# Performance work log

Measured on AMD Instinct MI355X. Metric: run time of the kernel, lower is better.

Reference implementation:

```python
import jax, jax.numpy as jnp
import numpy as np

B, T, C = 2, 1024, 2048
E, TOPK = 8, 2
F_MOE = 1408
F_SHARED = 5632


def setup_inputs() -> dict:
    key = jax.random.key(0)
    ks = jax.random.split(key, 9)
    s = 0.02
    return {
        "x": jax.random.normal(ks[0], (B, T, C), dtype=jnp.float32),
        "gate_w": jax.random.normal(ks[1], (E, C), dtype=jnp.float32) * s,
        "expert_fc1": jax.random.normal(ks[2], (E, F_MOE, C), dtype=jnp.float32) * s,
        "expert_fc2": jax.random.normal(ks[3], (E, F_MOE, C), dtype=jnp.float32) * s,
        "expert_proj": jax.random.normal(ks[4], (E, C, F_MOE), dtype=jnp.float32) * s,
        "shared_fc1": jax.random.normal(ks[5], (F_SHARED, C), dtype=jnp.float32) * s,
        "shared_fc2": jax.random.normal(ks[6], (F_SHARED, C), dtype=jnp.float32) * s,
        "shared_proj": jax.random.normal(ks[7], (C, F_SHARED), dtype=jnp.float32) * s,
        "shared_gate_w": jax.random.normal(ks[8], (1, C), dtype=jnp.float32) * s,
    }


def reference(x, gate_w, expert_fc1, expert_fc2, expert_proj,
              shared_fc1, shared_fc2, shared_proj, shared_gate_w):
    b, t, c = x.shape
    xf = x.reshape(-1, c)                                   # [N, C]
    n = xf.shape[0]

    # router: softmax in fp32, then top-k
    router = xf @ gate_w.T                                  # [N, E]
    probs = jax.nn.softmax(router.astype(jnp.float32), axis=1).astype(x.dtype)
    top_p, top_i = jax.lax.top_k(probs, TOPK)               # [N, k]

    # dense combine weights: prob where selected else 0 (top-k indices are distinct)
    combine = jnp.zeros((n, E), dtype=x.dtype).at[
        jnp.arange(n)[:, None], top_i].set(top_p)            # [N, E]

    # per-expert SwiGLU MLP, computed densely then weighted by combine
    h1 = jnp.einsum('nc,efc->enf', xf, expert_fc1)          # [E, N, F]
    h2 = jnp.einsum('nc,efc->enf', xf, expert_fc2)
    h = jax.nn.silu(h1) * h2
    out_e = jnp.einsum('enf,ecf->enc', h, expert_proj)      # [E, N, C]
    y = jnp.einsum('ne,enc->nc', combine, out_e)            # [N, C]

    # shared expert with sigmoid gate
    s1 = xf @ shared_fc1.T
    s2 = xf @ shared_fc2.T
    shared = (jax.nn.silu(s1) * s2) @ shared_proj.T         # [N, C]
    y = y + jax.nn.sigmoid(xf @ shared_gate_w.T) * shared
    return y.reshape(b, t, c)
```

## Files before the change

kernel.cpp:

```cpp
#include <hip/hip_runtime.h>
#include <hip/hip_bf16.h>
#include <math.h>
#include <stdint.h>

#define N_TOK   2048
#define C_DIM   2048
#define E_NUM   8
#define F_MOE   1408
#define F_SH    5632
#define SLOTS   4096
#define PADROWS 4608

typedef __bf16 bf16;
typedef __bf16 bf16x8 __attribute__((ext_vector_type(8)));
typedef __bf16 bf16x4 __attribute__((ext_vector_type(4)));
typedef float  f32x4  __attribute__((ext_vector_type(4)));

__device__ __forceinline__ f32x4 mfma16(bf16x8 a, bf16x8 b, f32x4 c) {
    return __builtin_amdgcn_mfma_f32_16x16x32_bf16(a, b, c, 0, 0, 0);
}
__device__ __forceinline__ void gload16(const void* g, void* l) {
    __builtin_amdgcn_global_load_lds(
        (const __attribute__((address_space(1))) void*)g,
        (__attribute__((address_space(3))) void*)l, 16, 0, 0);
}
#define RAWBAR()  asm volatile("s_barrier" ::: "memory")
#define VMCNT12() asm volatile("s_waitcnt vmcnt(12)" ::: "memory")
#define VMCNT8()  asm volatile("s_waitcnt vmcnt(8)" ::: "memory")
#define VMCNT4()  asm volatile("s_waitcnt vmcnt(4)" ::: "memory")
#define VMCNT0()  asm volatile("s_waitcnt vmcnt(0)" ::: "memory")

__global__ void router_kernel(const float* __restrict__ x,
                              const float* __restrict__ gate_w,
                              const float* __restrict__ sgate_w,
                              int* __restrict__ slotexp,
                              float* __restrict__ slotp,
                              float* __restrict__ sig)
{
    const int n   = blockIdx.x;
    const int tid = threadIdx.x;
    const float* xr = x + (size_t)n * C_DIM;
    const int c0 = tid * 8;

    float xv[8];
#pragma unroll
    for (int j = 0; j < 8; ++j) xv[j] = xr[c0 + j];

    float dots[9];
#pragma unroll
    for (int e = 0; e < 9; ++e) {
        const float* wr = (e < 8) ? (gate_w + (size_t)e * C_DIM) : sgate_w;
        float p = 0.f;
#pragma unroll
        for (int j = 0; j < 8; ++j) p += xv[j] * wr[c0 + j];
#pragma unroll
        for (int off = 32; off > 0; off >>= 1) p += __shfl_down(p, off);
        dots[e] = p;
    }

    __shared__ float red[4][9];
    const int wid = tid >> 6, lane = tid & 63;
    if (lane == 0) {
#pragma unroll
        for (int e = 0; e < 9; ++e) red[wid][e] = dots[e];
    }
    __syncthreads();
    if (tid == 0) {
        float l[9];
#pragma unroll
        for (int e = 0; e < 9; ++e)
            l[e] = red[0][e] + red[1][e] + red[2][e] + red[3][e];
        float mx = l[0];
#pragma unroll
        for (int e = 1; e < 8; ++e) mx = fmaxf(mx, l[e]);
        float p[8], s = 0.f;
#pragma unroll
        for (int e = 0; e < 8; ++e) { p[e] = expf(l[e] - mx); s += p[e]; }
        const float inv = 1.f / s;
#pragma unroll
        for (int e = 0; e < 8; ++e) p[e] *= inv;
        int i1 = 0;
#pragma unroll
        for (int e = 1; e < 8; ++e) if (p[e] > p[i1]) i1 = e;
        int i2 = (i1 == 0) ? 1 : 0;
#pragma unroll
        for (int e = 0; e < 8; ++e) if (e != i1 && p[e] > p[i2]) i2 = e;
        slotexp[2 * n]     = i1;  slotp[2 * n]     = p[i1];
        slotexp[2 * n + 1] = i2;  slotp[2 * n + 1] = p[i2];
        sig[n] = 1.f / (1.f + expf(-l[8]));
    }
}

__global__ void scatter_kernel(const int* __restrict__ slotexp,
                               int* __restrict__ counts, int* __restrict__ bases,
                               int* __restrict__ pos_of, int* __restrict__ row_token)
{
    const int tid = threadIdx.x;
    const int w = tid >> 6, lane = tid & 63;
    __shared__ int cnt[E_NUM], base[E_NUM];

    int run = 0;
    for (int s0 = 0; s0 < SLOTS; s0 += 64) {
        int e = slotexp[s0 + lane];
        unsigned long long m = __ballot(e == w);
        run += __popcll(m);
    }
    if (lane == 0) cnt[w] = run;
    __syncthreads();
    if (tid == 0) {
        int b = 0;
        for (int e = 0; e < E_NUM; ++e) { base[e] = b; b += cnt[e]; }
    }
    __syncthreads();
    run = 0;
    for (int s0 = 0; s0 < SLOTS; s0 += 64) {
        const int s = s0 + lane;
        const int e = slotexp[s];
        unsigned long long m = __ballot(e == w);
        if (e == w) {
            const unsigned long long lt = (lane == 0) ? 0ull : (~0ull >> (64 - lane));
            const int pos = base[w] + run + __popcll(m & lt);
            pos_of[s]      = pos;
            row_token[pos] = s >> 1;
        }
        run += __popcll(m);
    }
    if (lane == 0) { counts[w] = cnt[w]; bases[w] = base[w]; }
}

struct CvtArgs {
    const float* in[5];
    bf16*        out[5];
    int          cum[6];
};

__global__ void cvt_all_kernel(CvtArgs a)
{
    int b = blockIdx.x;
    int s = 0;
#pragma unroll
    for (int k = 1; k < 5; ++k) s += (b >= a.cum[k]);
    const size_t base = (size_t)(b - a.cum[s]) * 8192;
    const float* in = a.in[s];
    bf16* out = a.out[s];
    const int t4 = threadIdx.x * 4;
    f32x4 v[8];
#pragma unroll
    for (int c = 0; c < 8; ++c)
        v[c] = __builtin_nontemporal_load((const f32x4*)(in + base + c * 1024 + t4));
#pragma unroll
    for (int c = 0; c < 8; ++c) {
        bf16x4 o;
#pragma unroll
        for (int j = 0; j < 4; ++j) o[j] = (bf16)v[c][j];
        __builtin_nontemporal_store(o, (bf16x4*)(out + base + c * 1024 + t4));
    }
}

__global__ void gather_kernel(const bf16* __restrict__ Xs,
                              const int* __restrict__ row_token,
                              bf16* __restrict__ Xg)
{
    const int pos = blockIdx.x;
    const int t   = row_token[pos];
    const bf16x8* s = (const bf16x8*)(Xs + (size_t)t * C_DIM);
    bf16x8*       d = (bf16x8*)(Xg + (size_t)pos * C_DIM);
    d[threadIdx.x] = s[threadIdx.x];
}

template<bool DUAL, int KSPLIT>
__device__ __forceinline__ void gemm_body(
    const bf16* __restrict__ A, int lda,
    const bf16* __restrict__ B1g, const bf16* __restrict__ B2g, size_t strideB,
    bf16* __restrict__ OUTh, bf16* __restrict__ OUTq, int ldo, size_t strideOut,
    int base, int cnt, int e, int yt, int nt, int kp, int K, char* lds)
{
    const int KT = (K / 64) / KSPLIT;
    const int H  = 2 * KT;

    const int m0 = base + yt * 256;
    const int tid = threadIdx.x;
    const int w = tid >> 6, lane = tid & 63;

    const int l3  = lane >> 3;
    const int chS = (lane & 7) ^ l3;
    const int hiS = chS >> 2, ccS = chS & 3;
    const int rl  = w * 16 + 2 * l3 + hiS;
    const size_t lda2 = (size_t)lda * 2, K2 = (size_t)K * 2;
    const size_t kpoff = (size_t)kp * KT * 128;

    const char* aSrc0 = (const char*)A + (size_t)(m0 + rl)       * lda2 + ccS * 16 + kpoff;
    const char* aSrc1 = (const char*)A + (size_t)(m0 + 128 + rl) * lda2 + ccS * 16 + kpoff;
    const bf16* B1 = B1g + (size_t)e * strideB;
    const char* bSrc0;
    const char* bSrc1;
    if constexpr (DUAL) {
        const bf16* B2 = B2g + (size_t)e * strideB;
        bSrc0 = (const char*)B1 + (size_t)(nt * 128 + rl) * K2 + ccS * 16 + kpoff;
        bSrc1 = (const char*)B2 + (size_t)(nt * 128 + rl) * K2 + ccS * 16 + kpoff;
    } else {
        bSrc0 = (const char*)B1 + (size_t)(nt * 256 + rl)       * K2 + ccS * 16 + kpoff;
        bSrc1 = (const char*)B1 + (size_t)(nt * 256 + 128 + rl) * K2 + ccS * 16 + kpoff;
    }
    char* ldsw = lds + w * 1024;

    auto issue = [&](int h, int buf) {
        const size_t ko = (size_t)(h >> 1) * 128 + (size_t)(h & 1) * 64;
        char* d = ldsw + buf * 32768;
        gload16(aSrc0 + ko, d);
        gload16(aSrc1 + ko, d + 8192);
        gload16(bSrc0 + ko, d + 16384);
        gload16(bSrc1 + ko, d + 24576);
    };

    const int wm = w >> 2, wn = w & 3;
    const int fr = lane & 15, fq = lane >> 4;
    const int chRd = (((fr & 1) << 2) | fq) ^ ((fr >> 1) & 7);
    uint32_t aOff[8], bOff[4];
#pragma unroll
    for (int m = 0; m < 8; ++m)
        aOff[m] = (uint32_t)((wm * 64 + m * 8 + (fr >> 1)) * 128 + chRd * 16);
#pragma unroll
    for (int n = 0; n < 4; ++n) {
        int rp;
        if constexpr (DUAL)
            rp = (n < 2) ? (wn * 16 + n * 8) : (64 + wn * 16 + (n - 2) * 8);
        else
            rp = wn * 32 + n * 8;
        rp += (fr >> 1);
        bOff[n] = (uint32_t)(16384 + rp * 128 + chRd * 16);
    }

    f32x4 acc[8][4] = {};

    auto compute_half = [&](int buf) {
        const char* LB = lds + buf * 32768;
        bf16x8 af[4], ag[4], bf[4];
#pragma unroll
        for (int n = 0; n < 4; ++n) bf[n] = *(const bf16x8*)(LB + bOff[n]);
#pragma unroll
        for (int m = 0; m < 4; ++m) af[m] = *(const bf16x8*)(LB + aOff[m]);
#pragma unroll
        for (int m = 0; m < 4; ++m) ag[m] = *(const bf16x8*)(LB + aOff[4 + m]);
        __builtin_amdgcn_s_setprio(1);
#pragma unroll
        for (int m = 0; m < 4; ++m)
#pragma unroll
            for (int n = 0; n < 4; ++n)
                acc[m][n] = mfma16(af[m], bf[n], acc[m][n]);
#pragma unroll
        for (int m = 0; m < 4; ++m)
#pragma unroll
            for (int n = 0; n < 4; ++n)
                acc[4 + m][n] = mfma16(ag[m], bf[n], acc[4 + m][n]);
        __builtin_amdgcn_s_setprio(0);
    };

    issue(0, 0); issue(1, 1); issue(2, 2); issue(3, 3);

    int cur = 0, wr = 4;
    for (int h = 0; h < H - 4; ++h) {
        VMCNT12();
        RAWBAR();
        issue(h + 4, wr);
        compute_half(cur);
        cur = (cur == 4) ? 0 : cur + 1;
        wr  = (wr  == 4) ? 0 : wr  + 1;
    }
    VMCNT12(); RAWBAR(); compute_half(cur); cur = (cur == 4) ? 0 : cur + 1;
    VMCNT8();  RAWBAR(); compute_half(cur); cur = (cur == 4) ? 0 : cur + 1;
    VMCNT4();  RAWBAR(); compute_half(cur); cur = (cur == 4) ? 0 : cur + 1;
    VMCNT0();  RAWBAR(); compute_half(cur);

    const int rb0 = m0 + wm * 128;
    const int rend = base + cnt;
#pragma unroll
    for (int m = 0; m < 8; ++m) {
#pragma unroll
        for (int j = 0; j < 4; ++j) {
            const int grow = rb0 + m * 16 + fq * 4 + j;
            if (grow >= rend) continue;
            if constexpr (DUAL) {
#pragma unroll
                for (int n = 0; n < 2; ++n) {
                    const int gcol = nt * 128 + wn * 32 + n * 16 + fr;
                    const float h1 = acc[m][n][j];
                    const float h2 = acc[m][n + 2][j];
                    OUTh[(size_t)grow * ldo + gcol] =
                        (bf16)(h1 / (1.f + expf(-h1)) * h2);
                }
            } else {
                bf16* O = OUTq + (size_t)kp * strideOut;
#pragma unroll
                for (int n = 0; n < 4; ++n) {
                    const int gcol = nt * 256 + wn * 64 + n * 16 + fr;
                    O[(size_t)grow * ldo + gcol] = (bf16)acc[m][n][j];
                }
            }
        }
    }
}

template<bool DUAL, bool GROUPED, int KSPLIT>
__global__ __launch_bounds__(512, 1)
void gemm8(const bf16* __restrict__ A, int lda,
           const bf16* __restrict__ B1g, const bf16* __restrict__ B2g,
           size_t strideB,
           bf16* __restrict__ OUTh, bf16* __restrict__ OUTq, int ldo,
           size_t strideOut,
           const int* __restrict__ bases, const int* __restrict__ counts,
           int K)
{
    __shared__ char lds[163840];
    int e, yt, nt, kp, base, cnt;
    if constexpr (GROUPED) {
        e = blockIdx.x; yt = blockIdx.y; nt = blockIdx.z; kp = 0;
        base = bases[e]; cnt = counts[e];
        if (yt * 256 >= cnt) return;
    } else {
        nt = blockIdx.x; yt = blockIdx.y; kp = (KSPLIT > 1) ? blockIdx.z : 0;
        e = 0; base = 0; cnt = N_TOK;
    }
    gemm_body<DUAL, KSPLIT>(A, lda, B1g, B2g, strideB, OUTh, OUTq, ldo,
                            strideOut, base, cnt, e, yt, nt, kp, K, lds);
}

#define FC0_TILES 352
#define FC_TILES  1760
#define CVT_EP_BLKS 1408
#define CVT_SP_BLKS 704

__global__ __launch_bounds__(512, 1)
void gemm_fc(const bf16* __restrict__ Xs, const bf16* __restrict__ Xg,
             const bf16* __restrict__ Wsfc1, const bf16* __restrict__ Wsfc2,
             const bf16* __restrict__ Wefc1, const bf16* __restrict__ Wefc2,
             bf16* __restrict__ Hs, bf16* __restrict__ Hm,
             const float* __restrict__ eproj, const float* __restrict__ sproj,
             bf16* __restrict__ Weproj, bf16* __restrict__ Wsproj,
             const int* __restrict__ bases, const int* __restrict__ counts)
{
    __shared__ char lds[163840];
    const int id = blockIdx.x;
    if (id < FC0_TILES) {
        const int nt = id % 44, yt = id / 44;
        gemm_body<true, 1>(Xs, C_DIM, Wsfc1, Wsfc2, 0, Hs, nullptr, F_SH, 0,
                           0, N_TOK, 0, yt, nt, 0, C_DIM, lds);
    } else if (id < FC_TILES) {
        const int lid = id - FC0_TILES;
        const int e = lid & 7, yt = (lid >> 3) & 15, nt = lid >> 7;
        const int base = bases[e], cnt = counts[e];
        if (yt * 256 >= cnt) return;
        gemm_body<true, 1>(Xg, C_DIM, Wefc1, Wefc2, (size_t)F_MOE * C_DIM,
                           Hm, nullptr, F_MOE, 0,
                           base, cnt, e, yt, nt, 0, C_DIM, lds);
    } else {
        const int cid = id - FC_TILES;
        const float* in;
        bf16* out;
        size_t base;
        if (cid < CVT_EP_BLKS) { in = eproj; out = Weproj; base = (size_t)cid * 16384; }
        else { in = sproj; out = Wsproj; base = (size_t)(cid - CVT_EP_BLKS) * 16384; }
        const int t4 = threadIdx.x * 4;
        f32x4 v[8];
#pragma unroll
        for (int c = 0; c < 8; ++c)
            v[c] = __builtin_nontemporal_load((const f32x4*)(in + base + c * 2048 + t4));
#pragma unroll
        for (int c = 0; c < 8; ++c) {
            bf16x4 o;
#pragma unroll
            for (int j = 0; j < 4; ++j) o[j] = (bf16)v[c][j];
            __builtin_nontemporal_store(o, (bf16x4*)(out + base + c * 2048 + t4));
        }
    }
}

__global__ void combine_kernel(const bf16* __restrict__ SP,
                               const bf16* __restrict__ EP,
                               const int* __restrict__ pos_of,
                               const float* __restrict__ slotp,
                               const float* __restrict__ sig,
                               float* __restrict__ y)
{
    const int n  = blockIdx.x;
    const int p0 = pos_of[2 * n], p1 = pos_of[2 * n + 1];
    const float w0 = slotp[2 * n], w1 = slotp[2 * n + 1], sg = sig[n];
    const size_t PS = (size_t)N_TOK * C_DIM;
    const size_t cidx = (size_t)n * C_DIM + threadIdx.x * 8;

    bf16x8 s0 = *(const bf16x8*)(SP + cidx);
    bf16x8 s1 = *(const bf16x8*)(SP + cidx + PS);
    bf16x8 s2 = *(const bf16x8*)(SP + cidx + 2 * PS);
    bf16x8 s3 = *(const bf16x8*)(SP + cidx + 3 * PS);
    bf16x8 a0 = *(const bf16x8*)(EP + (size_t)p0 * C_DIM + threadIdx.x * 8);
    bf16x8 a1 = *(const bf16x8*)(EP + (size_t)p1 * C_DIM + threadIdx.x * 8);

    float out[8];
#pragma unroll
    for (int j = 0; j < 8; ++j) {
        const float ssum = (float)s0[j] + (float)s1[j] + (float)s2[j] + (float)s3[j];
        out[j] = sg * ssum + w0 * (float)a0[j] + w1 * (float)a1[j];
    }
    f32x4 o0, o1;
#pragma unroll
    for (int j = 0; j < 4; ++j) { o0[j] = out[j]; o1[j] = out[4 + j]; }
    *(f32x4*)(y + cidx)     = o0;
    *(f32x4*)(y + cidx + 4) = o1;
}

extern "C" void kernel_launch(void* const* d_in, const int* in_sizes, int n_in,
                              void* d_out, int out_size, void* d_ws, size_t ws_size,
                              hipStream_t stream)
{
    const float* x     = (const float*)d_in[0];
    const float* gatew = (const float*)d_in[1];
    const float* efc1  = (const float*)d_in[2];
    const float* efc2  = (const float*)d_in[3];
    const float* eproj = (const float*)d_in[4];
    const float* sfc1  = (const float*)d_in[5];
    const float* sfc2  = (const float*)d_in[6];
    const float* sproj = (const float*)d_in[7];
    const float* sgate = (const float*)d_in[8];
    float* y = (float*)d_out;

    char* w = (char*)d_ws;
    size_t off = 0;
    auto take = [&](size_t bytes) {
        char* p = w + off;
        off = (off + bytes + 255) & ~(size_t)255;
        return p;
    };
    int*   counts    = (int*)  take(E_NUM * 4);
    int*   bases     = (int*)  take(E_NUM * 4);
    int*   slotexp   = (int*)  take(SLOTS * 4);
    float* slotp     = (float*)take(SLOTS * 4);
    int*   pos_of    = (int*)  take(SLOTS * 4);
    int*   row_token = (int*)  take(PADROWS * 4);
    float* sig       = (float*)take(N_TOK * 4);
    bf16*  Xs        = (bf16*) take((size_t)N_TOK   * C_DIM * 2);
    bf16*  Xg        = (bf16*) take((size_t)PADROWS * C_DIM * 2);
    bf16*  Hs        = (bf16*) take((size_t)N_TOK   * F_SH  * 2);
    bf16*  Hm        = (bf16*) take((size_t)PADROWS * F_MOE * 2);
    bf16*  SP        = (bf16*) take((size_t)4 * N_TOK * C_DIM * 2);
    bf16*  EP        = (bf16*) take((size_t)PADROWS * C_DIM * 2);
    bf16*  Wefc1     = (bf16*) take((size_t)E_NUM * F_MOE * C_DIM * 2);
    bf16*  Wefc2     = (bf16*) take((size_t)E_NUM * F_MOE * C_DIM * 2);
    bf16*  Weproj    = (bf16*) take((size_t)E_NUM * C_DIM * F_MOE * 2);
    bf16*  Wsfc1     = (bf16*) take((size_t)F_SH * C_DIM * 2);
    bf16*  Wsfc2     = (bf16*) take((size_t)F_SH * C_DIM * 2);
    bf16*  Wsproj    = (bf16*) take((size_t)C_DIM * F_SH * 2);
    (void)ws_size; (void)in_sizes; (void)n_in; (void)out_size;

    CvtArgs ca;
    const int nbx  = (N_TOK * C_DIM) / 8192;
    const int nbe  = (E_NUM * F_MOE * C_DIM) / 8192;
    const int nbs  = (F_SH * C_DIM) / 8192;
    ca.in[0] = x;     ca.out[0] = Xs;
    ca.in[1] = efc1;  ca.out[1] = Wefc1;
    ca.in[2] = efc2;  ca.out[2] = Wefc2;
    ca.in[3] = sfc1;  ca.out[3] = Wsfc1;
    ca.in[4] = sfc2;  ca.out[4] = Wsfc2;
    ca.cum[0] = 0;
    ca.cum[1] = nbx;
    ca.cum[2] = nbx + nbe;
    ca.cum[3] = nbx + 2 * nbe;
    ca.cum[4] = nbx + 2 * nbe + nbs;
    ca.cum[5] = nbx + 2 * nbe + 2 * nbs;
    cvt_all_kernel<<<ca.cum[5], 256, 0, stream>>>(ca);

    router_kernel<<<N_TOK, 256, 0, stream>>>(x, gatew, sgate, slotexp, slotp, sig);
    scatter_kernel<<<1, 512, 0, stream>>>(slotexp, counts, bases, pos_of, row_token);
    gather_kernel<<<SLOTS, 256, 0, stream>>>(Xs, row_token, Xg);

    gemm_fc<<<FC_TILES + CVT_EP_BLKS + CVT_SP_BLKS, 512, 0, stream>>>(
        Xs, Xg, Wsfc1, Wsfc2, Wefc1, Wefc2, Hs, Hm,
        eproj, sproj, Weproj, Wsproj, bases, counts);

    gemm8<false, false, 4><<<dim3(C_DIM / 256, N_TOK / 256, 4), 512, 0, stream>>>(
        Hs, F_SH, Wsproj, nullptr, 0, nullptr, SP, C_DIM, (size_t)N_TOK * C_DIM,
        nullptr, nullptr, F_SH);

    gemm8<false, true, 1><<<dim3(E_NUM, SLOTS / 256, C_DIM / 256), 512, 0, stream>>>(
        Hm, F_MOE, Weproj, nullptr, (size_t)C_DIM * F_MOE, nullptr, EP, C_DIM, 0,
        bases, counts, F_MOE);

    combine_kernel<<<N_TOK, 256, 0, stream>>>(SP, EP, pos_of, slotp, sig, y);
}
```

Baseline: 408.6 us.

## Merge preprocessing kernels and fuse shared/expert projection GEMMs into one launch

The x bf16 conversion now shares a launch with the router, and the fc weight conversions share a launch with the scatter step (one block does the scatter while the rest convert, using larger 512-thread blocks). The shared-expert and routed-expert projection GEMMs become a single kernel that picks its tile from the block index. This removes several kernel launches and the tail/idle gaps between them, letting independent work overlap. In exchange the weight conversion now runs after the router instead of alongside it, and the grouped GEMM still launches many blocks that exit early.

```diff
diff --git a/kernel.cpp b/kernel.cpp
--- a/kernel.cpp
+++ b/kernel.cpp
@@ -30,14 +30,32 @@
 #define VMCNT4()  asm volatile("s_waitcnt vmcnt(4)" ::: "memory")
 #define VMCNT0()  asm volatile("s_waitcnt vmcnt(0)" ::: "memory")
 
-__global__ void router_kernel(const float* __restrict__ x,
-                              const float* __restrict__ gate_w,
-                              const float* __restrict__ sgate_w,
-                              int* __restrict__ slotexp,
-                              float* __restrict__ slotp,
-                              float* __restrict__ sig)
-{
-    const int n   = blockIdx.x;
+__global__ void cvtx_router_kernel(const float* __restrict__ x,
+                                   bf16* __restrict__ Xs,
+                                   const float* __restrict__ gate_w,
+                                   const float* __restrict__ sgate_w,
+                                   int* __restrict__ slotexp,
+                                   float* __restrict__ slotp,
+                                   float* __restrict__ sig)
+{
+    const int id = blockIdx.x;
+    if (id < 512) {
+        const size_t base = (size_t)id * 8192;
+        const int t4 = threadIdx.x * 4;
+        f32x4 v[8];
+#pragma unroll
+        for (int c = 0; c < 8; ++c)
+            v[c] = __builtin_nontemporal_load((const f32x4*)(x + base + c * 1024 + t4));
+#pragma unroll
+        for (int c = 0; c < 8; ++c) {
+            bf16x4 o;
+#pragma unroll
+            for (int j = 0; j < 4; ++j) o[j] = (bf16)v[c][j];
+            __builtin_nontemporal_store(o, (bf16x4*)(Xs + base + c * 1024 + t4));
+        }
+        return;
+    }
+    const int n   = id - 512;
     const int tid = threadIdx.x;
     const float* xr = x + (size_t)n * C_DIM;
     const int c0 = tid * 8;
@@ -91,69 +109,72 @@
     }
 }
 
-__global__ void scatter_kernel(const int* __restrict__ slotexp,
-                               int* __restrict__ counts, int* __restrict__ bases,
-                               int* __restrict__ pos_of, int* __restrict__ row_token)
-{
-    const int tid = threadIdx.x;
-    const int w = tid >> 6, lane = tid & 63;
-    __shared__ int cnt[E_NUM], base[E_NUM];
-
-    int run = 0;
-    for (int s0 = 0; s0 < SLOTS; s0 += 64) {
-        int e = slotexp[s0 + lane];
-        unsigned long long m = __ballot(e == w);
-        run += __popcll(m);
-    }
-    if (lane == 0) cnt[w] = run;
-    __syncthreads();
-    if (tid == 0) {
-        int b = 0;
-        for (int e = 0; e < E_NUM; ++e) { base[e] = b; b += cnt[e]; }
-    }
-    __syncthreads();
-    run = 0;
-    for (int s0 = 0; s0 < SLOTS; s0 += 64) {
-        const int s = s0 + lane;
-        const int e = slotexp[s];
-        unsigned long long m = __ballot(e == w);
-        if (e == w) {
-            const unsigned long long lt = (lane == 0) ? 0ull : (~0ull >> (64 - lane));
-            const int pos = base[w] + run + __popcll(m & lt);
-            pos_of[s]      = pos;
-            row_token[pos] = s >> 1;
-        }
-        run += __popcll(m);
-    }
-    if (lane == 0) { counts[w] = cnt[w]; bases[w] = base[w]; }
-}
-
-struct CvtArgs {
-    const float* in[5];
-    bf16*        out[5];
-    int          cum[6];
-};
-
-__global__ void cvt_all_kernel(CvtArgs a)
-{
-    int b = blockIdx.x;
-    int s = 0;
-#pragma unroll
-    for (int k = 1; k < 5; ++k) s += (b >= a.cum[k]);
-    const size_t base = (size_t)(b - a.cum[s]) * 8192;
-    const float* in = a.in[s];
-    bf16* out = a.out[s];
+#define CVT_EFC_BLKS 1408
+#define CVT_SFC_BLKS 704
+
+__global__ __launch_bounds__(512)
+void scatter_cvt_kernel(const int* __restrict__ slotexp,
+                        int* __restrict__ counts, int* __restrict__ bases,
+                        int* __restrict__ pos_of, int* __restrict__ row_token,
+                        const float* __restrict__ efc1, const float* __restrict__ efc2,
+                        const float* __restrict__ sfc1, const float* __restrict__ sfc2,
+                        bf16* __restrict__ Wefc1, bf16* __restrict__ Wefc2,
+                        bf16* __restrict__ Wsfc1, bf16* __restrict__ Wsfc2)
+{
+    const int id = blockIdx.x;
+    if (id == 0) {
+        const int tid = threadIdx.x;
+        const int w = tid >> 6, lane = tid & 63;
+        __shared__ int cnt[E_NUM], base[E_NUM];
+
+        int run = 0;
+        for (int s0 = 0; s0 < SLOTS; s0 += 64) {
+            int e = slotexp[s0 + lane];
+            unsigned long long m = __ballot(e == w);
+            run += __popcll(m);
+        }
+        if (lane == 0) cnt[w] = run;
+        __syncthreads();
+        if (tid == 0) {
+            int b = 0;
+            for (int e = 0; e < E_NUM; ++e) { base[e] = b; b += cnt[e]; }
+        }
+        __syncthreads();
+        run = 0;
+        for (int s0 = 0; s0 < SLOTS; s0 += 64) {
+            const int s = s0 + lane;
+            const int e = slotexp[s];
+            unsigned long long m = __ballot(e == w);
+            if (e == w) {
+                const unsigned long long lt = (lane == 0) ? 0ull : (~0ull >> (64 - lane));
+                const int pos = base[w] + run + __popcll(m & lt);
+                pos_of[s]      = pos;
+                row_token[pos] = s >> 1;
+            }
+            run += __popcll(m);
+        }
+        if (lane == 0) { counts[w] = cnt[w]; bases[w] = base[w]; }
+        return;
+    }
+    int cid = id - 1;
+    const float* in;
+    bf16* out;
+    if (cid < CVT_EFC_BLKS) { in = efc1; out = Wefc1; }
+    else if (cid < 2 * CVT_EFC_BLKS) { in = efc2; out = Wefc2; cid -= CVT_EFC_BLKS; }
+    else if (cid < 2 * CVT_EFC_BLKS + CVT_SFC_BLKS) { in = sfc1; out = Wsfc1; cid -= 2 * CVT_EFC_BLKS; }
+    else { in = sfc2; out = Wsfc2; cid -= 2 * CVT_EFC_BLKS + CVT_SFC_BLKS; }
+    const size_t base = (size_t)cid * 16384;
     const int t4 = threadIdx.x * 4;
     f32x4 v[8];
 #pragma unroll
     for (int c = 0; c < 8; ++c)
-        v[c] = __builtin_nontemporal_load((const f32x4*)(in + base + c * 1024 + t4));
+        v[c] = __builtin_nontemporal_load((const f32x4*)(in + base + c * 2048 + t4));
 #pragma unroll
     for (int c = 0; c < 8; ++c) {
         bf16x4 o;
 #pragma unroll
         for (int j = 0; j < 4; ++j) o[j] = (bf16)v[c][j];
-        __builtin_nontemporal_store(o, (bf16x4*)(out + base + c * 1024 + t4));
+        __builtin_nontemporal_store(o, (bf16x4*)(out + base + c * 2048 + t4));
     }
 }
 
@@ -299,30 +320,6 @@
             }
         }
     }
-}
-
-template<bool DUAL, bool GROUPED, int KSPLIT>
-__global__ __launch_bounds__(512, 1)
-void gemm8(const bf16* __restrict__ A, int lda,
-           const bf16* __restrict__ B1g, const bf16* __restrict__ B2g,
-           size_t strideB,
-           bf16* __restrict__ OUTh, bf16* __restrict__ OUTq, int ldo,
-           size_t strideOut,
-           const int* __restrict__ bases, const int* __restrict__ counts,
-           int K)
-{
-    __shared__ char lds[163840];
-    int e, yt, nt, kp, base, cnt;
-    if constexpr (GROUPED) {
-        e = blockIdx.x; yt = blockIdx.y; nt = blockIdx.z; kp = 0;
-        base = bases[e]; cnt = counts[e];
-        if (yt * 256 >= cnt) return;
-    } else {
-        nt = blockIdx.x; yt = blockIdx.y; kp = (KSPLIT > 1) ? blockIdx.z : 0;
-        e = 0; base = 0; cnt = N_TOK;
-    }
-    gemm_body<DUAL, KSPLIT>(A, lda, B1g, B2g, strideB, OUTh, OUTq, ldo,
-                            strideOut, base, cnt, e, yt, nt, kp, K, lds);
 }
 
 #define FC0_TILES 352
@@ -372,6 +369,32 @@
             for (int j = 0; j < 4; ++j) o[j] = (bf16)v[c][j];
             __builtin_nontemporal_store(o, (bf16x4*)(out + base + c * 2048 + t4));
         }
+    }
+}
+
+#define PROJ0_TILES 256
+
+__global__ __launch_bounds__(512, 1)
+void gemm_proj(const bf16* __restrict__ Hs, const bf16* __restrict__ Hm,
+               const bf16* __restrict__ Wsproj, const bf16* __restrict__ Weproj,
+               bf16* __restrict__ SP, bf16* __restrict__ EP,
+               const int* __restrict__ bases, const int* __restrict__ counts)
+{
+    __shared__ char lds[163840];
+    const int id = blockIdx.x;
+    if (id < PROJ0_TILES) {
+        const int nt = id & 7, yt = (id >> 3) & 7, kp = id >> 6;
+        gemm_body<false, 4>(Hs, F_SH, Wsproj, nullptr, 0, nullptr, SP, C_DIM,
+                            (size_t)N_TOK * C_DIM,
+                            0, N_TOK, 0, yt, nt, kp, F_SH, lds);
+    } else {
+        const int lid = id - PROJ0_TILES;
+        const int e = lid & 7, yt = (lid >> 3) & 15, nt = lid >> 7;
+        const int base = bases[e], cnt = counts[e];
+        if (yt * 256 >= cnt) return;
+        gemm_body<false, 1>(Hm, F_MOE, Weproj, nullptr, (size_t)C_DIM * F_MOE,
+                            nullptr, EP, C_DIM, 0,
+                            base, cnt, e, yt, nt, 0, F_MOE, lds);
     }
 }
 
@@ -451,38 +474,21 @@
     bf16*  Wsproj    = (bf16*) take((size_t)C_DIM * F_SH * 2);
     (void)ws_size; (void)in_sizes; (void)n_in; (void)out_size;
 
-    CvtArgs ca;
-    const int nbx  = (N_TOK * C_DIM) / 8192;
-    const int nbe  = (E_NUM * F_MOE * C_DIM) / 8192;
-    const int nbs  = (F_SH * C_DIM) / 8192;
-    ca.in[0] = x;     ca.out[0] = Xs;
-    ca.in[1] = efc1;  ca.out[1] = Wefc1;
-    ca.in[2] = efc2;  ca.out[2] = Wefc2;
-    ca.in[3] = sfc1;  ca.out[3] = Wsfc1;
-    ca.in[4] = sfc2;  ca.out[4] = Wsfc2;
-    ca.cum[0] = 0;
-    ca.cum[1] = nbx;
-    ca.cum[2] = nbx + nbe;
-    ca.cum[3] = nbx + 2 * nbe;
-    ca.cum[4] = nbx + 2 * nbe + nbs;
-    ca.cum[5] = nbx + 2 * nbe + 2 * nbs;
-    cvt_all_kernel<<<ca.cum[5], 256, 0, stream>>>(ca);
-
-    router_kernel<<<N_TOK, 256, 0, stream>>>(x, gatew, sgate, slotexp, slotp, sig);
-    scatter_kernel<<<1, 512, 0, stream>>>(slotexp, counts, bases, pos_of, row_token);
+    cvtx_router_kernel<<<512 + N_TOK, 256, 0, stream>>>(
+        x, Xs, gatew, sgate, slotexp, slotp, sig);
+
+    scatter_cvt_kernel<<<1 + 2 * CVT_EFC_BLKS + 2 * CVT_SFC_BLKS, 512, 0, stream>>>(
+        slotexp, counts, bases, pos_of, row_token,
+        efc1, efc2, sfc1, sfc2, Wefc1, Wefc2, Wsfc1, Wsfc2);
+
     gather_kernel<<<SLOTS, 256, 0, stream>>>(Xs, row_token, Xg);
 
     gemm_fc<<<FC_TILES + CVT_EP_BLKS + CVT_SP_BLKS, 512, 0, stream>>>(
         Xs, Xg, Wsfc1, Wsfc2, Wefc1, Wefc2, Hs, Hm,
         eproj, sproj, Weproj, Wsproj, bases, counts);
 
-    gemm8<false, false, 4><<<dim3(C_DIM / 256, N_TOK / 256, 4), 512, 0, stream>>>(
-        Hs, F_SH, Wsproj, nullptr, 0, nullptr, SP, C_DIM, (size_t)N_TOK * C_DIM,
-        nullptr, nullptr, F_SH);
-
-    gemm8<false, true, 1><<<dim3(E_NUM, SLOTS / 256, C_DIM / 256), 512, 0, stream>>>(
-        Hm, F_MOE, Weproj, nullptr, (size_t)C_DIM * F_MOE, nullptr, EP, C_DIM, 0,
-        bases, counts, F_MOE);
+    gemm_proj<<<PROJ0_TILES + E_NUM * (SLOTS / 256) * (C_DIM / 256), 512, 0, stream>>>(
+        Hs, Hm, Wsproj, Weproj, SP, EP, bases, counts);
 
     combine_kernel<<<N_TOK, 256, 0, stream>>>(SP, EP, pos_of, slotp, sig, y);
 }
```

After: 389.9 us. -4.6%, faster.
